# Optimization experiments

Measured on AMD Instinct MI355X. Metric: run time of the kernel, lower is better.

The kernel has to match this reference:

```python
import jax, jax.numpy as jnp
import numpy as np

B, S, E, H = 4, 2048, 1024, 16
D = E // H  # head dim = 64

def setup_inputs() -> dict:
    key = jax.random.key(0)
    k1, k2, k3 = jax.random.split(key, 3)
    scale = 0.02
    return {
        "x": jax.random.normal(k1, (B, S, E), dtype=jnp.float32),
        "W_qkv": jax.random.normal(k2, (E, 3 * E), dtype=jnp.float32) * scale,
        "b_qkv": jnp.zeros((3 * E,), dtype=jnp.float32),
        "W_o": jax.random.normal(k3, (E, E), dtype=jnp.float32) * scale,
        "b_o": jnp.zeros((E,), dtype=jnp.float32),
    }

def reference(x, W_qkv, b_qkv, W_o, b_o):
    # dropout is identity in eval mode
    qkv = x @ W_qkv + b_qkv                      # [B, S, 3E]
    q, k, v = jnp.split(qkv, 3, axis=-1)          # each [B, S, E]
    def split_heads(t):
        return t.reshape(B, S, H, D).transpose(0, 2, 1, 3)  # [B, H, S, D]
    q, k, v = split_heads(q), split_heads(k), split_heads(v)
    scores = jnp.einsum("bhsd,bhtd->bhst", q, k) / jnp.sqrt(jnp.float32(D))
    causal = jnp.tril(jnp.ones((S, S), dtype=bool))
    scores = jnp.where(causal[None, None], scores, jnp.float32(-jnp.inf))
    attn = jax.nn.softmax(scores, axis=-1)        # [B, H, S, S]
    out = jnp.einsum("bhst,bhtd->bhsd", attn, v)  # [B, H, S, D]
    out = out.transpose(0, 2, 1, 3).reshape(B, S, E)
    return out @ W_o + b_o
```

## Files before the change

kernel.cpp:

```cpp
#include <hip/hip_runtime.h>
#include <stdint.h>

typedef __bf16 bf16_t;
typedef __bf16 bf16x8 __attribute__((ext_vector_type(8)));
typedef float f32x4 __attribute__((ext_vector_type(4)));

#define LOG2E 1.44269504088896340736f

__device__ __forceinline__ float fexp2(float x) {
#if __has_builtin(__builtin_amdgcn_exp2f)
    return __builtin_amdgcn_exp2f(x);
#else
    return exp2f(x);
#endif
}

__device__ __forceinline__ void gld_lds16(const bf16_t* g, bf16_t* l) {
    __builtin_amdgcn_global_load_lds(
        (__attribute__((address_space(1))) void*)(bf16_t*)g,
        (__attribute__((address_space(3))) void*)l,
        16, 0, 0);
}

__global__ __launch_bounds__(256) void prep_k(
    const float* __restrict__ x, bf16_t* __restrict__ xb,
    const float* __restrict__ Wqkv, bf16_t* __restrict__ wqkvT,
    const float* __restrict__ Wo, bf16_t* __restrict__ woT)
{
    __shared__ float t[32][33];
    const int tid = threadIdx.x;
    int blk = blockIdx.x;
    if (blk < 8192) {
        int i = blk * 1024 + tid * 4;
        float4 v = *(const float4*)(x + i);
        union { bf16_t b[4]; uint2 u; } u;
        u.b[0] = (bf16_t)v.x; u.b[1] = (bf16_t)v.y; u.b[2] = (bf16_t)v.z; u.b[3] = (bf16_t)v.w;
        *(uint2*)(xb + i) = u.u;
        return;
    }
    const float* in; bf16_t* out; int C, bx, by;
    if (blk < 11264) { blk -= 8192; in = Wqkv; out = wqkvT; C = 3072; bx = blk % 96; by = blk / 96; }
    else             { blk -= 11264; in = Wo;   out = woT;   C = 1024; bx = blk % 32; by = blk / 32; }
    const int R = 1024;
    const int tx = tid & 31, ty = tid >> 5;
    const int c0 = bx * 32, r0 = by * 32;
    #pragma unroll
    for (int j = 0; j < 32; j += 8)
        t[ty + j][tx] = in[(size_t)(r0 + ty + j) * C + c0 + tx];
    __syncthreads();
    #pragma unroll
    for (int j = 0; j < 32; j += 8)
        out[(size_t)(c0 + ty + j) * R + r0 + tx] = (bf16_t)t[tx][ty + j];
}

__device__ __forceinline__ void gemm_body_pipe(
    const bf16_t* __restrict__ A, const bf16_t* __restrict__ Bt,
    bf16_t* Al, bf16_t* Bl, f32x4 (&acc)[4][4], int m0, int n0)
{
    const int tid = threadIdx.x;
    const int w = tid >> 6, lane = tid & 63;
    const int l15 = lane & 15, quad = lane >> 4;
    const int wm = w >> 2, wn = w & 3;

    const int srow = lane >> 3;
    const int scg = ((lane & 7) ^ srow) * 8;
    const bf16_t* Ag = A  + (size_t)(m0 + w * 16 + srow) * 1024 + scg;
    const bf16_t* Bg = Bt + (size_t)(n0 + w * 32 + srow) * 1024 + scg;

    const int rc0 = (quad ^ (l15 & 7)) * 8;
    const int rc1 = ((quad + 4) ^ (l15 & 7)) * 8;

    auto stage0 = [&](int kt, int ss) {
        gld_lds16(Ag + kt * 64,                       Al + ss * 8192  + (w * 16) * 64);
        gld_lds16(Ag + kt * 64 + (size_t)8 * 1024,    Al + ss * 8192  + (w * 16 + 8) * 64);
        gld_lds16(Bg + kt * 64,                       Bl + ss * 16384 + (w * 32) * 64);
    };
    auto stage1 = [&](int kt, int ss) {
        gld_lds16(Bg + kt * 64 + (size_t)8 * 1024,    Bl + ss * 16384 + (w * 32 + 8) * 64);
        gld_lds16(Bg + kt * 64 + (size_t)16 * 1024,   Bl + ss * 16384 + (w * 32 + 16) * 64);
        gld_lds16(Bg + kt * 64 + (size_t)24 * 1024,   Bl + ss * 16384 + (w * 32 + 24) * 64);
    };

    stage0(0, 0); stage1(0, 0);
    stage0(1, 1); stage1(1, 1);
    asm volatile("s_waitcnt vmcnt(6)" ::: "memory");
    __builtin_amdgcn_s_barrier();

    int cs = 0, ss = 2;
    for (int t = 0; t < 16; ++t) {
        const bf16_t* Ab = Al + cs * 8192;
        const bf16_t* Bb = Bl + cs * 16384;
        {
            bf16x8 af[4], bfr[4];
            #pragma unroll
            for (int mi = 0; mi < 4; mi++)
                af[mi] = *(const bf16x8*)(Ab + (wm * 64 + mi * 16 + l15) * 64 + rc0);
            #pragma unroll
            for (int ni = 0; ni < 4; ni++)
                bfr[ni] = *(const bf16x8*)(Bb + (wn * 64 + ni * 16 + l15) * 64 + rc0);
            if (t < 14) stage0(t + 2, ss);
            __builtin_amdgcn_s_barrier();
            __builtin_amdgcn_s_setprio(1);
            #pragma unroll
            for (int mi = 0; mi < 4; mi++)
                #pragma unroll
                for (int ni = 0; ni < 4; ni++)
                    acc[mi][ni] = __builtin_amdgcn_mfma_f32_16x16x32_bf16(
                        af[mi], bfr[ni], acc[mi][ni], 0, 0, 0);
            __builtin_amdgcn_s_setprio(0);
            __builtin_amdgcn_s_barrier();
        }
        {
            bf16x8 af[4], bfr[4];
            #pragma unroll
            for (int mi = 0; mi < 4; mi++)
                af[mi] = *(const bf16x8*)(Ab + (wm * 64 + mi * 16 + l15) * 64 + rc1);
            #pragma unroll
            for (int ni = 0; ni < 4; ni++)
                bfr[ni] = *(const bf16x8*)(Bb + (wn * 64 + ni * 16 + l15) * 64 + rc1);
            if (t < 14) {
                stage1(t + 2, ss);
                asm volatile("s_waitcnt vmcnt(6)" ::: "memory");
            } else if (t == 14) {
                asm volatile("s_waitcnt vmcnt(0)" ::: "memory");
            }
            __builtin_amdgcn_s_barrier();
            __builtin_amdgcn_s_setprio(1);
            #pragma unroll
            for (int mi = 0; mi < 4; mi++)
                #pragma unroll
                for (int ni = 0; ni < 4; ni++)
                    acc[mi][ni] = __builtin_amdgcn_mfma_f32_16x16x32_bf16(
                        af[mi], bfr[ni], acc[mi][ni], 0, 0, 0);
            __builtin_amdgcn_s_setprio(0);
            __builtin_amdgcn_s_barrier();
        }
        cs = (cs == 2) ? 0 : cs + 1;
        ss = (ss == 2) ? 0 : ss + 1;
    }
}

__global__ __launch_bounds__(512) void gemm_qkv_k(
    const bf16_t* __restrict__ X, const bf16_t* __restrict__ WT,
    const float* __restrict__ bias,
    bf16_t* __restrict__ Qb, bf16_t* __restrict__ Kb, bf16_t* __restrict__ VTb)
{
    __shared__ bf16_t Al[3 * 128 * 64];
    __shared__ bf16_t Bl[3 * 256 * 64];
    const int tid = threadIdx.x;
    const int lane = tid & 63, w = tid >> 6;
    const int l15 = lane & 15, quad = lane >> 4;
    const int wm = w >> 2, wn = w & 3;
    const int n0 = blockIdx.x * 256;
    const int m0 = blockIdx.y * 128;

    f32x4 acc[4][4];
    #pragma unroll
    for (int mi = 0; mi < 4; mi++)
        #pragma unroll
        for (int ni = 0; ni < 4; ni++) acc[mi][ni] = (f32x4){0.f, 0.f, 0.f, 0.f};

    gemm_body_pipe(WT, X, Al, Bl, acc, m0, n0);

    const float QSCALE = 0.125f * LOG2E;
    const int region = m0 >> 10;
    #pragma unroll
    for (int mi = 0; mi < 4; mi++) {
        const int mbase = m0 + wm * 64 + mi * 16 + quad * 4;
        const float4 bia = *(const float4*)(bias + mbase);
        const float ba[4] = {bia.x, bia.y, bia.z, bia.w};
        const int col = mbase & 1023;
        const int h = col >> 6, dbase = col & 63;
        #pragma unroll
        for (int ni = 0; ni < 4; ni++) {
            const int n = n0 + wn * 64 + ni * 16 + l15;
            const int b = n >> 11, s = n & 2047;
            if (region == 0) {
                union { bf16_t bv[4]; uint2 u; } u;
                #pragma unroll
                for (int r = 0; r < 4; r++)
                    u.bv[r] = (bf16_t)((acc[mi][ni][r] + ba[r]) * QSCALE);
                *(uint2*)(Qb + (((size_t)b * 16 + h) * 2048 + s) * 64 + dbase) = u.u;
            } else if (region == 1) {
                union { bf16_t bv[4]; uint2 u; } u;
                #pragma unroll
                for (int r = 0; r < 4; r++)
                    u.bv[r] = (bf16_t)(acc[mi][ni][r] + ba[r]);
                *(uint2*)(Kb + (((size_t)b * 16 + h) * 2048 + s) * 64 + dbase) = u.u;
            } else {
                bf16_t* dst = VTb + (((size_t)b * 16 + h) * 64 + dbase) * 2048 + s;
                #pragma unroll
                for (int r = 0; r < 4; r++)
                    dst[(size_t)r * 2048] = (bf16_t)(acc[mi][ni][r] + ba[r]);
            }
        }
    }
}

__global__ __launch_bounds__(256) void attn_k(
    const bf16_t* __restrict__ Qb, const bf16_t* __restrict__ Kb,
    const bf16_t* __restrict__ VTb, bf16_t* __restrict__ Ob)
{
    __shared__ bf16_t Kl[64 * 64];
    __shared__ bf16_t Vl[64 * 64];
    __shared__ bf16_t Pl[4][32 * 72];

    const int tid = threadIdx.x;
    const int w = tid >> 6, lane = tid & 63;
    const int l15 = lane & 15, quad = lane >> 4;
    const int idx = blockIdx.x;
    const int qt = 15 - (idx >> 6);
    const int bh = idx & 63;
    const int b = bh >> 4, h = bh & 15;
    const int q0 = qt * 128;

    const bf16_t* Qp = Qb + (size_t)bh * 2048 * 64;
    const bf16_t* Kp = Kb + (size_t)bh * 2048 * 64;
    const bf16_t* Vp = VTb + (size_t)bh * 64 * 2048;

    const int srow = w * 16 + (lane >> 3);
    const int scol = ((lane & 7) ^ ((lane >> 3) & 7)) * 8;
    const int rc0 = (quad ^ (l15 & 7)) * 8;
    const int rc1 = ((quad + 4) ^ (l15 & 7)) * 8;

    bf16x8 aq[2][2];
    #pragma unroll
    for (int g = 0; g < 2; g++) {
        const int qrow = q0 + w * 32 + g * 16 + l15;
        aq[g][0] = *(const bf16x8*)(Qp + (size_t)qrow * 64 + quad * 8);
        aq[g][1] = *(const bf16x8*)(Qp + (size_t)qrow * 64 + 32 + quad * 8);
    }

    bf16x8 vone;
    #pragma unroll
    for (int j = 0; j < 8; j++) vone[j] = (bf16_t)1.0f;

    f32x4 o[2][4];
    #pragma unroll
    for (int g = 0; g < 2; g++)
        #pragma unroll
        for (int ni = 0; ni < 4; ni++) o[g][ni] = (f32x4){0.f, 0.f, 0.f, 0.f};
    f32x4 lacc[2];
    lacc[0] = (f32x4){0.f, 0.f, 0.f, 0.f};
    lacc[1] = (f32x4){0.f, 0.f, 0.f, 0.f};

    for (int kv0 = 0; kv0 <= q0 + 64; kv0 += 64) {
        __syncthreads();
        gld_lds16(Kp + (size_t)(kv0 + srow) * 64 + scol, Kl + (w * 16) * 64);
        gld_lds16(Kp + (size_t)(kv0 + srow + 8) * 64 + scol, Kl + (w * 16 + 8) * 64);
        gld_lds16(Vp + (size_t)srow * 2048 + kv0 + scol, Vl + (w * 16) * 64);
        gld_lds16(Vp + (size_t)(srow + 8) * 2048 + kv0 + scol, Vl + (w * 16 + 8) * 64);
        __syncthreads();

        bf16x8 ak[4][2], bv[4][2];
        #pragma unroll
        for (int ni = 0; ni < 4; ni++) {
            ak[ni][0] = *(const bf16x8*)(Kl + (ni * 16 + l15) * 64 + rc0);
            ak[ni][1] = *(const bf16x8*)(Kl + (ni * 16 + l15) * 64 + rc1);
        }
        #pragma unroll
        for (int ni = 0; ni < 4; ni++) {
            bv[ni][0] = *(const bf16x8*)(Vl + (ni * 16 + l15) * 64 + rc0);
            bv[ni][1] = *(const bf16x8*)(Vl + (ni * 16 + l15) * 64 + rc1);
        }

        #pragma unroll
        for (int g = 0; g < 2; g++) {
            const int qloc = w * 32 + g * 16 + l15;
            f32x4 sv[4];
            #pragma unroll
            for (int ni = 0; ni < 4; ni++) {
                f32x4 z = (f32x4){0.f, 0.f, 0.f, 0.f};
                z = __builtin_amdgcn_mfma_f32_16x16x32_bf16(ak[ni][0], aq[g][0], z, 0, 0, 0);
                z = __builtin_amdgcn_mfma_f32_16x16x32_bf16(ak[ni][1], aq[g][1], z, 0, 0, 0);
                sv[ni] = z;
            }

            if (kv0 >= q0) {
                const int koff = kv0 - q0;
                #pragma unroll
                for (int ni = 0; ni < 4; ni++)
                    #pragma unroll
                    for (int r = 0; r < 4; r++)
                        if (koff + ni * 16 + quad * 4 + r > qloc) sv[ni][r] = -INFINITY;
            }

            #pragma unroll
            for (int ni = 0; ni < 4; ni++) {
                union { bf16_t bvv[4]; uint2 u; } pk;
                #pragma unroll
                for (int r = 0; r < 4; r++) pk.bvv[r] = (bf16_t)fexp2(sv[ni][r]);
                *(uint2*)(&Pl[w][(g * 16 + l15) * 72 + ni * 16 + quad * 4]) = pk.u;
            }

            bf16x8 pa0 = *(const bf16x8*)(&Pl[w][(g * 16 + l15) * 72 + quad * 8]);
            bf16x8 pa1 = *(const bf16x8*)(&Pl[w][(g * 16 + l15) * 72 + 32 + quad * 8]);
            #pragma unroll
            for (int ni = 0; ni < 4; ni++) {
                o[g][ni] = __builtin_amdgcn_mfma_f32_16x16x32_bf16(bv[ni][0], pa0, o[g][ni], 0, 0, 0);
                o[g][ni] = __builtin_amdgcn_mfma_f32_16x16x32_bf16(bv[ni][1], pa1, o[g][ni], 0, 0, 0);
            }
            lacc[g] = __builtin_amdgcn_mfma_f32_16x16x32_bf16(vone, pa0, lacc[g], 0, 0, 0);
            lacc[g] = __builtin_amdgcn_mfma_f32_16x16x32_bf16(vone, pa1, lacc[g], 0, 0, 0);
        }
    }

    #pragma unroll
    for (int g = 0; g < 2; g++) {
        const float inv = 1.0f / lacc[g][0];
        const int s = q0 + w * 32 + g * 16 + l15;
        bf16_t* obase = Ob + ((size_t)b * 2048 + s) * 1024 + h * 64;
        #pragma unroll
        for (int ni = 0; ni < 4; ni++) {
            union { bf16_t bvv[4]; uint2 u; } u;
            #pragma unroll
            for (int r = 0; r < 4; r++) u.bvv[r] = (bf16_t)(o[g][ni][r] * inv);
            *(uint2*)(obase + ni * 16 + quad * 4) = u.u;
        }
    }
}

__global__ __launch_bounds__(512) void gemm_out_k(
    const bf16_t* __restrict__ O, const bf16_t* __restrict__ WT,
    const float* __restrict__ bias, float* __restrict__ out)
{
    __shared__ bf16_t Al[3 * 128 * 64];
    __shared__ bf16_t Bl[3 * 256 * 64];
    const int tid = threadIdx.x;
    const int lane = tid & 63, w = tid >> 6;
    const int l15 = lane & 15, quad = lane >> 4;
    const int wm = w >> 2, wn = w & 3;
    const int n0 = blockIdx.x * 256;
    const int m0 = blockIdx.y * 128;

    f32x4 acc[4][4];
    #pragma unroll
    for (int mi = 0; mi < 4; mi++)
        #pragma unroll
        for (int ni = 0; ni < 4; ni++) acc[mi][ni] = (f32x4){0.f, 0.f, 0.f, 0.f};

    gemm_body_pipe(WT, O, Al, Bl, acc, m0, n0);

    #pragma unroll
    for (int mi = 0; mi < 4; mi++) {
        const int mbase = m0 + wm * 64 + mi * 16 + quad * 4;
        const float4 bia = *(const float4*)(bias + mbase);
        #pragma unroll
        for (int ni = 0; ni < 4; ni++) {
            const int n = n0 + wn * 64 + ni * 16 + l15;
            float4 v;
            v.x = acc[mi][ni][0] + bia.x;
            v.y = acc[mi][ni][1] + bia.y;
            v.z = acc[mi][ni][2] + bia.z;
            v.w = acc[mi][ni][3] + bia.w;
            *(float4*)(out + (size_t)n * 1024 + mbase) = v;
        }
    }
}


extern "C" void kernel_launch(void* const* d_in, const int* in_sizes, int n_in,
                              void* d_out, int out_size, void* d_ws, size_t ws_size,
                              hipStream_t stream) {
    const float* x     = (const float*)d_in[0];
    const float* W_qkv = (const float*)d_in[1];
    const float* b_qkv = (const float*)d_in[2];
    const float* W_o   = (const float*)d_in[3];
    const float* b_o   = (const float*)d_in[4];
    float* out = (float*)d_out;

    char* ws = (char*)d_ws;
    size_t off = 0;
    auto alloc = [&](size_t bytes) -> void* {
        void* p = ws + off;
        off += (bytes + 255) & ~(size_t)255;
        return p;
    };
    bf16_t* xb    = (bf16_t*)alloc((size_t)8192 * 1024 * 2);
    bf16_t* wqkvT = (bf16_t*)alloc((size_t)3072 * 1024 * 2);
    bf16_t* woT   = (bf16_t*)alloc((size_t)1024 * 1024 * 2);
    bf16_t* Qb    = (bf16_t*)alloc((size_t)8192 * 1024 * 2);
    bf16_t* Kb    = (bf16_t*)alloc((size_t)8192 * 1024 * 2);
    bf16_t* VTb   = (bf16_t*)alloc((size_t)8192 * 1024 * 2);
    bf16_t* Ob    = xb;

    prep_k<<<12288, 256, 0, stream>>>(x, xb, W_qkv, wqkvT, W_o, woT);
    gemm_qkv_k<<<dim3(32, 24), 512, 0, stream>>>(xb, wqkvT, b_qkv, Qb, Kb, VTb);
    attn_k<<<1024, 256, 0, stream>>>(Qb, Kb, VTb, Ob);
    gemm_out_k<<<dim3(32, 8), 512, 0, stream>>>(Ob, woT, b_o, out);
}
```

Baseline: 244.5 us.

## Double-buffer K/V tiles in attention kernel to overlap loads with compute

Splits the K and V shared-memory tiles into two buffers and prefetches the next 64-row KV tile with global_load_lds while the current tile is consumed. An explicit vmcnt wait lets the older loads complete while the newer ones stay in flight. This is meant to hide global-memory latency behind the MFMA and softmax work. It doubles K/V LDS usage, which may reduce occupancy, and it relies on hand-written waitcnt and barrier ordering.

Result: no change. 245.6 us (+0.4%).

```diff
diff --git a/kernel.cpp b/kernel.cpp
--- a/kernel.cpp
+++ b/kernel.cpp
@@ -201,8 +201,8 @@
     const bf16_t* __restrict__ Qb, const bf16_t* __restrict__ Kb,
     const bf16_t* __restrict__ VTb, bf16_t* __restrict__ Ob)
 {
-    __shared__ bf16_t Kl[64 * 64];
-    __shared__ bf16_t Vl[64 * 64];
+    __shared__ bf16_t Kl[2][64 * 64];
+    __shared__ bf16_t Vl[2][64 * 64];
     __shared__ bf16_t Pl[4][32 * 72];
 
     const int tid = threadIdx.x;
@@ -244,24 +244,43 @@
     lacc[0] = (f32x4){0.f, 0.f, 0.f, 0.f};
     lacc[1] = (f32x4){0.f, 0.f, 0.f, 0.f};
 
-    for (int kv0 = 0; kv0 <= q0 + 64; kv0 += 64) {
-        __syncthreads();
-        gld_lds16(Kp + (size_t)(kv0 + srow) * 64 + scol, Kl + (w * 16) * 64);
-        gld_lds16(Kp + (size_t)(kv0 + srow + 8) * 64 + scol, Kl + (w * 16 + 8) * 64);
-        gld_lds16(Vp + (size_t)srow * 2048 + kv0 + scol, Vl + (w * 16) * 64);
-        gld_lds16(Vp + (size_t)(srow + 8) * 2048 + kv0 + scol, Vl + (w * 16 + 8) * 64);
-        __syncthreads();
+    const int nkv = (q0 >> 6) + 2;
+
+    auto stage = [&](int kvt, int buf) {
+        const int kv0 = kvt << 6;
+        gld_lds16(Kp + (size_t)(kv0 + srow) * 64 + scol, Kl[buf] + (w * 16) * 64);
+        gld_lds16(Kp + (size_t)(kv0 + srow + 8) * 64 + scol, Kl[buf] + (w * 16 + 8) * 64);
+        gld_lds16(Vp + (size_t)srow * 2048 + kv0 + scol, Vl[buf] + (w * 16) * 64);
+        gld_lds16(Vp + (size_t)(srow + 8) * 2048 + kv0 + scol, Vl[buf] + (w * 16 + 8) * 64);
+    };
+
+    stage(0, 0);
+
+    for (int t = 0; t < nkv; ++t) {
+        const int buf = t & 1;
+        const int kv0 = t << 6;
+        __builtin_amdgcn_s_barrier();
+        if (t + 1 < nkv) {
+            stage(t + 1, buf ^ 1);
+            asm volatile("s_waitcnt vmcnt(4)" ::: "memory");
+        } else {
+            asm volatile("s_waitcnt vmcnt(0)" ::: "memory");
+        }
+        __builtin_amdgcn_s_barrier();
+
+        const bf16_t* Kb_ = Kl[buf];
+        const bf16_t* Vb_ = Vl[buf];
 
         bf16x8 ak[4][2], bv[4][2];
         #pragma unroll
         for (int ni = 0; ni < 4; ni++) {
-            ak[ni][0] = *(const bf16x8*)(Kl + (ni * 16 + l15) * 64 + rc0);
-            ak[ni][1] = *(const bf16x8*)(Kl + (ni * 16 + l15) * 64 + rc1);
+            ak[ni][0] = *(const bf16x8*)(Kb_ + (ni * 16 + l15) * 64 + rc0);
+            ak[ni][1] = *(const bf16x8*)(Kb_ + (ni * 16 + l15) * 64 + rc1);
         }
         #pragma unroll
         for (int ni = 0; ni < 4; ni++) {
-            bv[ni][0] = *(const bf16x8*)(Vl + (ni * 16 + l15) * 64 + rc0);
-            bv[ni][1] = *(const bf16x8*)(Vl + (ni * 16 + l15) * 64 + rc1);
+            bv[ni][0] = *(const bf16x8*)(Vb_ + (ni * 16 + l15) * 64 + rc0);
+            bv[ni][1] = *(const bf16x8*)(Vb_ + (ni * 16 + l15) * 64 + rc1);
         }
 
         #pragma unroll
```
